# Kernel optimization log

Measured on AMD Instinct MI355X. Metric: run time of the kernel, lower is better.

The kernel has to match this reference:

```python
import jax, jax.numpy as jnp
from jax import lax
import numpy as np

WIDTH = 3.0        # tool half-width (voxels)
SIGMA = 1.0        # soft mask edge (voxels)
BLUR_SIGMA = 1.5   # post-deposit isotropic blur sigma (voxels)
EPS = 1e-8


def _gauss_blur(x, sigma):
    """Separable Gaussian blur over the last two axes of x: [B, X, Y]."""
    radius = int(3 * sigma)
    t = jnp.arange(-radius, radius + 1, dtype=x.dtype)
    k = jnp.exp(-0.5 * (t / sigma) ** 2)
    k = k / k.sum()
    x4 = x[:, None]                      # [B,1,X,Y] NCHW
    kh = k.reshape(1, 1, -1, 1)
    x4 = lax.conv_general_dilated(x4, kh, (1, 1), 'SAME')
    kw = k.reshape(1, 1, 1, -1)
    x4 = lax.conv_general_dilated(x4, kw, (1, 1), 'SAME')
    return x4[:, 0]


def setup_inputs() -> dict:
    key = jax.random.key(0)
    k1, k2, k3 = jax.random.split(key, 3)
    B, H, W = 16, 1024, 1024
    occ = jax.random.uniform(k1, (B, H, W), dtype=jnp.float32)
    # push start/end points well inside the grid (voxel coordinates)
    action_start = jax.random.uniform(k2, (B, 3), minval=200.0, maxval=800.0, dtype=jnp.float32)
    action_end = action_start + jax.random.uniform(k3, (B, 3), minval=-150.0, maxval=150.0, dtype=jnp.float32)
    return {"occ": occ, "action_start": action_start, "action_end": action_end}


def reference(occ, action_start, action_end):
    # coordinate-convention transpose (see SplatPushModel docs)
    rho = jnp.swapaxes(occ, 1, 2)            # [B, X, Y]
    B, X, Y = rho.shape
    p0 = action_start[:, :2]                 # [B,2]
    p1 = action_end[:, :2]                   # [B,2]

    d = p1 - p0
    L = jnp.sqrt(jnp.sum(d * d, axis=-1) + EPS)      # [B] segment length
    u = d / L[:, None]                               # unit push direction
    n = jnp.stack([-u[:, 1], u[:, 0]], axis=-1)      # unit normal

    gx = jnp.arange(X, dtype=rho.dtype)[None, :, None]   # [1,X,1]
    gy = jnp.arange(Y, dtype=rho.dtype)[None, None, :]   # [1,1,Y]
    bc = lambda v: v[:, None, None]                      # [B] -> [B,1,1]

    # --- swept band: soft distance-to-segment mask ---
    rx = gx - bc(p0[:, 0])
    ry = gy - bc(p0[:, 1])
    t = jnp.clip(rx * bc(u[:, 0]) + ry * bc(u[:, 1]), 0.0, L[:, None, None])
    dx = rx - t * bc(u[:, 0])
    dy = ry - t * bc(u[:, 1])
    dist = jnp.sqrt(dx * dx + dy * dy + EPS)
    swept = jax.nn.sigmoid((WIDTH - dist) / SIGMA)       # [B,X,Y]

    m_swept = jnp.sum(rho * swept, axis=(1, 2))          # [B] mass to move
    pile_depth = m_swept / (2.0 * WIDTH)                 # [B]

    # --- landing zone probe (rectangle past p1) ---
    qx = gx - bc(p1[:, 0])
    qy = gy - bc(p1[:, 1])
    s = qx * bc(u[:, 0]) + qy * bc(u[:, 1])              # along-direction coord
    r = qx * bc(n[:, 0]) + qy * bc(n[:, 1])              # perpendicular coord
    lat = jax.nn.sigmoid((WIDTH - jnp.abs(r)) / SIGMA)
    probe = jax.nn.sigmoid(s / SIGMA) * jax.nn.sigmoid((bc(pile_depth) - s) / SIGMA) * lat
    existing = jnp.sum(rho * probe, axis=(1, 2))         # [B]
    extra = existing / (2.0 * WIDTH)                     # [B] forward extension

    # --- deposit band, shifted forward by extra_depth ---
    dep_mask = (jax.nn.sigmoid((s - bc(extra)) / SIGMA)
                * jax.nn.sigmoid((bc(extra) + bc(pile_depth) - s) / SIGMA)
                * lat)
    dep_norm = m_swept / (jnp.sum(dep_mask, axis=(1, 2)) + EPS)
    dep = dep_mask * dep_norm[:, None, None]             # mass-conserving deposit

    if BLUR_SIGMA > 0:
        dep = _gauss_blur(dep, BLUR_SIGMA)

    rho_new = rho * (1.0 - swept) + dep
    return jnp.swapaxes(rho_new, 1, 2)
```

## Files before the change

kernel.cpp:

```cpp
#include <hip/hip_runtime.h>
#include <math.h>

#define BB    16
#define HH    1024
#define WW    1024
#define EPSF  1e-8f
#define RAD   4
#define MARG  24.f
#define NB1   128
#define NB2   64
#define NB3   32
#define WMAX  128
#define FW    (WMAX + 16)

struct BlurK { float k[9]; };

__device__ __forceinline__ float sigf(float z) {
    z = fmaxf(fminf(z, 40.f), -40.f);
    return 1.f / (1.f + __expf(-z));
}

struct Geom { float p0x, p0y, p1x, p1y, L, ux, uy; };

__device__ __forceinline__ Geom load_geom(const float* as, const float* ae, int b) {
    Geom g;
    g.p0x = as[3 * b];  g.p0y = as[3 * b + 1];
    g.p1x = ae[3 * b];  g.p1y = ae[3 * b + 1];
    float dx = g.p1x - g.p0x, dy = g.p1y - g.p0y;
    g.L  = sqrtf(dx * dx + dy * dy + EPSF);
    g.ux = dx / g.L;  g.uy = dy / g.L;
    return g;
}

__device__ __forceinline__ float sweptf(const Geom& g, float x, float y) {
    float rx = x - g.p0x, ry = y - g.p0y;
    float t  = fminf(fmaxf(rx * g.ux + ry * g.uy, 0.f), g.L);
    float dx = rx - t * g.ux, dy = ry - t * g.uy;
    float dist = sqrtf(dx * dx + dy * dy + EPSF);
    return sigf(3.f - dist);
}

__device__ __forceinline__ void slat(const Geom& g, float x, float y, float& s, float& lat) {
    float qx = x - g.p1x, qy = y - g.p1y;
    s = qx * g.ux + qy * g.uy;
    float r = qx * (-g.uy) + qy * g.ux;
    lat = sigf(3.f - fabsf(r));
}

__device__ __forceinline__ void capsule_bbox(const Geom& g, float m,
                                             int& x0, int& x1, int& y0, int& y1) {
    x0 = max(0, (int)floorf(fminf(g.p0x, g.p1x) - m));
    x1 = min(WW - 1, (int)ceilf(fmaxf(g.p0x, g.p1x) + m));
    y0 = max(0, (int)floorf(fminf(g.p0y, g.p1y) - m));
    y1 = min(HH - 1, (int)ceilf(fmaxf(g.p0y, g.p1y) + m));
}

__device__ __forceinline__ void strip_bbox(const Geom& g, float s0, float s1, float m,
                                           int& x0, int& x1, int& y0, int& y1) {
    float xmin = 1e9f, xmax = -1e9f, ymin = 1e9f, ymax = -1e9f;
    #pragma unroll
    for (int i = 0; i < 4; i++) {
        float s = (i & 1) ? s1 : s0;
        float r = (i & 2) ? m : -m;
        float x = g.p1x + s * g.ux - r * g.uy;
        float y = g.p1y + s * g.uy + r * g.ux;
        xmin = fminf(xmin, x); xmax = fmaxf(xmax, x);
        ymin = fminf(ymin, y); ymax = fmaxf(ymax, y);
    }
    x0 = max(0, (int)floorf(xmin)); x1 = min(WW - 1, (int)ceilf(xmax));
    y0 = max(0, (int)floorf(ymin)); y1 = min(HH - 1, (int)ceilf(ymax));
}

__device__ __forceinline__ bool ivx(float a, float A, float B, float& lo, float& hi) {
    if (fabsf(a) < 1e-5f) return !(A > 0.f || B < 0.f);
    float l = A / a, h = B / a;
    if (a < 0.f) { float t = l; l = h; h = t; }
    lo = fmaxf(lo, l); hi = fminf(hi, h);
    return true;
}

__device__ __forceinline__ float brb256(float v, float* sm) {
    #pragma unroll
    for (int off = 32; off > 0; off >>= 1) v += __shfl_down(v, off);
    const int lane = threadIdx.x & 63, wid = threadIdx.x >> 6;
    if (lane == 0) sm[wid] = v;
    __syncthreads();
    float r = sm[0] + sm[1] + sm[2] + sm[3];
    __syncthreads();
    return r;
}

__global__ __launch_bounds__(256)
void k_main(const float* __restrict__ occ, const float* __restrict__ as,
            const float* __restrict__ ae, float* __restrict__ out,
            float* __restrict__ part1) {
    const int b = blockIdx.y, bx = blockIdx.x, tid = threadIdx.x;
    Geom g = load_geom(as, ae, b);
    const size_t ibase = (size_t)b << 20;
    const float4* src = (const float4*)(occ + ibase);
    float4*       dst = (float4*)(out + ibase);
    const int yb = bx * 8;
    const int base4 = bx * 2048 + tid;

    float4 v[8];
    #pragma unroll
    for (int k = 0; k < 8; k++) v[k] = src[base4 + k * 256];

    int cx0, cx1, cy0, cy1; capsule_bbox(g, MARG, cx0, cx1, cy0, cy1);
    const int x = tid << 2;
    float msum = 0.f;
    if (x + 3 >= cx0 && x <= cx1) {
        #pragma unroll
        for (int k = 0; k < 8; k++) {
            const int y = yb + k;
            if (y >= cy0 && y <= cy1) {
                const float fy = (float)y, fx = (float)x;
                const float s0 = sweptf(g, fx + 0.f, fy);
                const float s1 = sweptf(g, fx + 1.f, fy);
                const float s2 = sweptf(g, fx + 2.f, fy);
                const float s3 = sweptf(g, fx + 3.f, fy);
                msum += v[k].x * s0 + v[k].y * s1 + v[k].z * s2 + v[k].w * s3;
                v[k].x *= 1.f - s0; v[k].y *= 1.f - s1;
                v[k].z *= 1.f - s2; v[k].w *= 1.f - s3;
            }
        }
    }
    #pragma unroll
    for (int k = 0; k < 8; k++) dst[base4 + k * 256] = v[k];

    __shared__ float sm[4];
    const float bs = brb256(msum, sm);
    if (tid == 0) part1[b * NB1 + bx] = bs;
}

__global__ __launch_bounds__(256)
void k_existing(const float* __restrict__ occ, const float* __restrict__ as,
                const float* __restrict__ ae, const float* __restrict__ part1,
                float* __restrict__ part2) {
    const int b = blockIdx.y, bx = blockIdx.x, tid = threadIdx.x;
    __shared__ float sm[4];
    const float m_swept = brb256((tid < NB1) ? part1[b * NB1 + tid] : 0.f, sm);
    const float pile = m_swept * (1.f / 6.f);

    Geom g = load_geom(as, ae, b);
    int x0, x1, y0, y1; strip_bbox(g, -MARG, pile + MARG, MARG, x0, x1, y0, y1);
    const float* base = occ + ((size_t)b << 20);
    float sum = 0.f;
    for (int y = y0 + bx; y <= y1; y += NB2) {
        const float fy = (float)y;
        for (int x = x0 + tid; x <= x1; x += 256) {
            float s, lat; slat(g, (float)x, fy, s, lat);
            sum += base[((size_t)y << 10) + x] * sigf(s) * sigf(pile - s) * lat;
        }
    }
    const float bs = brb256(sum, sm);
    if (tid == 0) part2[b * NB2 + bx] = bs;
}

__global__ __launch_bounds__(256)
void k_summask(const float* __restrict__ as, const float* __restrict__ ae,
               const float* __restrict__ part1, const float* __restrict__ part2,
               float* __restrict__ part3) {
    const int b = blockIdx.y, bx = blockIdx.x, tid = threadIdx.x;
    __shared__ float sm[4];
    const float m_swept  = brb256((tid < NB1) ? part1[b * NB1 + tid] : 0.f, sm);
    const float existing = brb256((tid < NB2) ? part2[b * NB2 + tid] : 0.f, sm);
    const float pile  = m_swept * (1.f / 6.f);
    const float extra = existing * (1.f / 6.f);

    Geom g = load_geom(as, ae, b);
    int x0, x1, y0, y1;
    strip_bbox(g, extra - MARG, extra + pile + MARG, MARG, x0, x1, y0, y1);
    float sum = 0.f;
    for (int y = y0 + bx; y <= y1; y += NB2) {
        const float fy = (float)y;
        for (int x = x0 + tid; x <= x1; x += 256) {
            float s, lat; slat(g, (float)x, fy, s, lat);
            sum += sigf(s - extra) * sigf(extra + pile - s) * lat;
        }
    }
    const float bs = brb256(sum, sm);
    if (tid == 0) part3[b * NB2 + bx] = bs;
}

__global__ __launch_bounds__(256)
void k_dep(const float* __restrict__ as, const float* __restrict__ ae,
           const float* __restrict__ part1, const float* __restrict__ part2,
           const float* __restrict__ part3, float* __restrict__ out, BlurK wk) {
    const int b = blockIdx.y, bx = blockIdx.x, tid = threadIdx.x;
    __shared__ float sm[4];
    const float m_swept  = brb256((tid < NB1) ? part1[b * NB1 + tid] : 0.f, sm);
    const float existing = brb256((tid < NB2) ? part2[b * NB2 + tid] : 0.f, sm);
    const float summask  = brb256((tid < NB2) ? part3[b * NB2 + tid] : 0.f, sm);
    const float pile     = m_swept * (1.f / 6.f);
    const float extra    = existing * (1.f / 6.f);
    const float dep_norm = m_swept / (summask + EPSF);

    Geom g = load_geom(as, ae, b);
    int sx0, sx1, sy0, sy1;
    strip_bbox(g, extra - MARG, extra + pile + MARG, MARG, sx0, sx1, sy0, sy1);
    if (sx0 > sx1 || sy0 > sy1) return;
    float* outb = out + ((size_t)b << 20);

    __shared__ float draw[16][FW];
    __shared__ float hb[16][WMAX];

    const int nty = (sy1 - sy0) / 8 + 1;
    const float sA = extra - MARG, sB = extra + pile + MARG;

    for (int ty = bx; ty < nty; ty += NB3) {
        const int yt = sy0 + ty * 8;

        float xlo = 1e9f, xhi = -1e9f;
        #pragma unroll
        for (int r = 0; r < 16; r++) {
            const float dy = (float)(yt - RAD + r) - g.p1y;
            float lo = -1e9f, hi = 1e9f;
            bool ok = ivx(g.ux, sA - dy * g.uy, sB - dy * g.uy, lo, hi);
            ok = ok && ivx(-g.uy, -MARG - dy * g.ux, MARG - dy * g.ux, lo, hi);
            if (ok && lo <= hi) { xlo = fminf(xlo, lo); xhi = fmaxf(xhi, hi); }
        }
        const int csx0 = max(sx0, (int)floorf(xlo + g.p1x));
        const int csx1 = min(sx1, (int)ceilf(xhi + g.p1x));
        if (csx0 > csx1) continue;

        for (int cx = csx0 & ~3; cx <= csx1; cx += WMAX) {
            const int w = min(WMAX, csx1 - cx + 1);

            for (int i = tid; i < 16 * FW; i += 256) {
                const int ly = i / FW, lx = i - ly * FW;
                if (lx < w + 8) {
                    const int gy = yt - RAD + ly, gx = cx - RAD + lx;
                    float val = 0.f;
                    if ((unsigned)gx < WW && (unsigned)gy < HH) {
                        float s, lat; slat(g, (float)gx, (float)gy, s, lat);
                        val = sigf(s - extra) * sigf(extra + pile - s) * lat * dep_norm;
                    }
                    draw[ly][lx] = val;
                }
            }
            __syncthreads();

            for (int i = tid; i < 16 * WMAX; i += 256) {
                const int ly = i >> 7, lx = i & 127;
                if (lx < w) {
                    float acc = 0.f;
                    #pragma unroll
                    for (int j = 0; j < 9; j++) acc += wk.k[j] * draw[ly][lx + j];
                    hb[ly][lx] = acc;
                }
            }
            __syncthreads();

            for (int i = tid; i < 8 * WMAX; i += 256) {
                const int k = i >> 7, lx = i & 127;
                if (lx < w) {
                    float acc = 0.f;
                    #pragma unroll
                    for (int j = 0; j < 9; j++) acc += wk.k[j] * hb[k + j][lx];
                    draw[k][lx] = acc;
                }
            }
            __syncthreads();

            for (int i = tid; i < 8 * WMAX; i += 256) {
                const int k = i >> 7, lx = i & 127;
                const int gy = yt + k, gx = cx + lx;
                if (lx < w && (unsigned)gy < HH && (unsigned)gx < WW)
                    outb[((size_t)gy << 10) + gx] += draw[k][lx];
            }
            __syncthreads();
        }
    }
}

extern "C" void kernel_launch(void* const* d_in, const int* in_sizes, int n_in,
                              void* d_out, int out_size, void* d_ws, size_t ws_size,
                              hipStream_t stream) {
    const float* occ = (const float*)d_in[0];
    const float* as  = (const float*)d_in[1];
    const float* ae  = (const float*)d_in[2];
    float* out   = (float*)d_out;
    float* part1 = (float*)d_ws;
    float* part2 = part1 + BB * NB1;
    float* part3 = part2 + BB * NB2;

    BlurK wk;
    {
        float s = 0.f;
        for (int i = 0; i < 9; i++) {
            float t = (float)(i - RAD) / 1.5f;
            wk.k[i] = expf(-0.5f * t * t);
            s += wk.k[i];
        }
        for (int i = 0; i < 9; i++) wk.k[i] /= s;
    }

    k_main    <<<dim3(NB1, BB), 256, 0, stream>>>(occ, as, ae, out, part1);
    k_existing<<<dim3(NB2, BB), 256, 0, stream>>>(occ, as, ae, part1, part2);
    k_summask <<<dim3(NB2, BB), 256, 0, stream>>>(as, ae, part1, part2, part3);
    k_dep     <<<dim3(NB3, BB), 256, 0, stream>>>(as, ae, part1, part2, part3, out, wk);
}
```

Measured before the change: 136.3 us.

## Fuse existing-mass and mask-sum reductions into deposit kernel with per-row clipping

Merges the k_existing and k_summask reductions into k_dep, so every block of k_dep redundantly computes the landing-zone probe sum and the deposit-mask sum on its own. This removes two kernel launches and the partial-sum round trips through workspace memory. It also adds per-row x clipping of the rotated strip, so only pixels inside the band are visited rather than the whole axis-aligned bounding box. The cost is that 32 blocks per batch each repeat both reductions serially, which adds latency before the blur and deposit stage.

```diff
diff --git a/kernel.cpp b/kernel.cpp
--- a/kernel.cpp
+++ b/kernel.cpp
@@ -8,7 +8,6 @@
 #define RAD   4
 #define MARG  24.f
 #define NB1   128
-#define NB2   64
 #define NB3   32
 #define WMAX  128
 #define FW    (WMAX + 16)
@@ -77,6 +76,18 @@
     if (a < 0.f) { float t = l; l = h; h = t; }
     lo = fmaxf(lo, l); hi = fminf(hi, h);
     return true;
+}
+
+__device__ __forceinline__ bool row_clip(const Geom& g, float fy, float sA, float sB,
+                                         int& xa, int& xb) {
+    const float dy = fy - g.p1y;
+    float lo = -1e9f, hi = 1e9f;
+    bool ok = ivx(g.ux, sA - dy * g.uy, sB - dy * g.uy, lo, hi);
+    ok = ok && ivx(-g.uy, -MARG - dy * g.ux, MARG - dy * g.ux, lo, hi);
+    if (!ok || lo > hi) return false;
+    xa = max(0, (int)floorf(lo + g.p1x));
+    xb = min(WW - 1, (int)ceilf(hi + g.p1x));
+    return xa <= xb;
 }
 
 __device__ __forceinline__ float brb256(float v, float* sm) {
@@ -134,71 +145,49 @@
 }
 
 __global__ __launch_bounds__(256)
-void k_existing(const float* __restrict__ occ, const float* __restrict__ as,
-                const float* __restrict__ ae, const float* __restrict__ part1,
-                float* __restrict__ part2) {
+void k_dep(const float* __restrict__ occ, const float* __restrict__ as,
+           const float* __restrict__ ae, const float* __restrict__ part1,
+           float* __restrict__ out, BlurK wk) {
     const int b = blockIdx.y, bx = blockIdx.x, tid = threadIdx.x;
+    const int lane = tid & 63, wv = tid >> 6;
     __shared__ float sm[4];
+    Geom g = load_geom(as, ae, b);
+    const float* ob = occ + ((size_t)b << 20);
+
     const float m_swept = brb256((tid < NB1) ? part1[b * NB1 + tid] : 0.f, sm);
     const float pile = m_swept * (1.f / 6.f);
 
-    Geom g = load_geom(as, ae, b);
-    int x0, x1, y0, y1; strip_bbox(g, -MARG, pile + MARG, MARG, x0, x1, y0, y1);
-    const float* base = occ + ((size_t)b << 20);
+    int x0, x1, y0, y1;
+    strip_bbox(g, -MARG, pile + MARG, MARG, x0, x1, y0, y1);
     float sum = 0.f;
-    for (int y = y0 + bx; y <= y1; y += NB2) {
+    for (int y = y0 + wv; y <= y1; y += 4) {
         const float fy = (float)y;
-        for (int x = x0 + tid; x <= x1; x += 256) {
-            float s, lat; slat(g, (float)x, fy, s, lat);
-            sum += base[((size_t)y << 10) + x] * sigf(s) * sigf(pile - s) * lat;
-        }
-    }
-    const float bs = brb256(sum, sm);
-    if (tid == 0) part2[b * NB2 + bx] = bs;
-}
-
-__global__ __launch_bounds__(256)
-void k_summask(const float* __restrict__ as, const float* __restrict__ ae,
-               const float* __restrict__ part1, const float* __restrict__ part2,
-               float* __restrict__ part3) {
-    const int b = blockIdx.y, bx = blockIdx.x, tid = threadIdx.x;
-    __shared__ float sm[4];
-    const float m_swept  = brb256((tid < NB1) ? part1[b * NB1 + tid] : 0.f, sm);
-    const float existing = brb256((tid < NB2) ? part2[b * NB2 + tid] : 0.f, sm);
-    const float pile  = m_swept * (1.f / 6.f);
+        int xa, xb;
+        if (!row_clip(g, fy, -MARG, pile + MARG, xa, xb)) continue;
+        for (int xx = xa + lane; xx <= xb; xx += 64) {
+            float s, lat; slat(g, (float)xx, fy, s, lat);
+            sum += ob[((size_t)y << 10) + xx] * sigf(s) * sigf(pile - s) * lat;
+        }
+    }
+    const float existing = brb256(sum, sm);
     const float extra = existing * (1.f / 6.f);
 
-    Geom g = load_geom(as, ae, b);
-    int x0, x1, y0, y1;
-    strip_bbox(g, extra - MARG, extra + pile + MARG, MARG, x0, x1, y0, y1);
-    float sum = 0.f;
-    for (int y = y0 + bx; y <= y1; y += NB2) {
+    const float sA = extra - MARG, sB = extra + pile + MARG;
+    int sx0, sx1, sy0, sy1;
+    strip_bbox(g, sA, sB, MARG, sx0, sx1, sy0, sy1);
+    sum = 0.f;
+    for (int y = sy0 + wv; y <= sy1; y += 4) {
         const float fy = (float)y;
-        for (int x = x0 + tid; x <= x1; x += 256) {
-            float s, lat; slat(g, (float)x, fy, s, lat);
+        int xa, xb;
+        if (!row_clip(g, fy, sA, sB, xa, xb)) continue;
+        for (int xx = xa + lane; xx <= xb; xx += 64) {
+            float s, lat; slat(g, (float)xx, fy, s, lat);
             sum += sigf(s - extra) * sigf(extra + pile - s) * lat;
         }
     }
-    const float bs = brb256(sum, sm);
-    if (tid == 0) part3[b * NB2 + bx] = bs;
-}
-
-__global__ __launch_bounds__(256)
-void k_dep(const float* __restrict__ as, const float* __restrict__ ae,
-           const float* __restrict__ part1, const float* __restrict__ part2,
-           const float* __restrict__ part3, float* __restrict__ out, BlurK wk) {
-    const int b = blockIdx.y, bx = blockIdx.x, tid = threadIdx.x;
-    __shared__ float sm[4];
-    const float m_swept  = brb256((tid < NB1) ? part1[b * NB1 + tid] : 0.f, sm);
-    const float existing = brb256((tid < NB2) ? part2[b * NB2 + tid] : 0.f, sm);
-    const float summask  = brb256((tid < NB2) ? part3[b * NB2 + tid] : 0.f, sm);
-    const float pile     = m_swept * (1.f / 6.f);
-    const float extra    = existing * (1.f / 6.f);
+    const float summask = brb256(sum, sm);
     const float dep_norm = m_swept / (summask + EPSF);
 
-    Geom g = load_geom(as, ae, b);
-    int sx0, sx1, sy0, sy1;
-    strip_bbox(g, extra - MARG, extra + pile + MARG, MARG, sx0, sx1, sy0, sy1);
     if (sx0 > sx1 || sy0 > sy1) return;
     float* outb = out + ((size_t)b << 20);
 
@@ -206,7 +195,6 @@
     __shared__ float hb[16][WMAX];
 
     const int nty = (sy1 - sy0) / 8 + 1;
-    const float sA = extra - MARG, sB = extra + pile + MARG;
 
     for (int ty = bx; ty < nty; ty += NB3) {
         const int yt = sy0 + ty * 8;
@@ -282,8 +270,6 @@
     const float* ae  = (const float*)d_in[2];
     float* out   = (float*)d_out;
     float* part1 = (float*)d_ws;
-    float* part2 = part1 + BB * NB1;
-    float* part3 = part2 + BB * NB2;
 
     BlurK wk;
     {
@@ -296,8 +282,6 @@
         for (int i = 0; i < 9; i++) wk.k[i] /= s;
     }
 
-    k_main    <<<dim3(NB1, BB), 256, 0, stream>>>(occ, as, ae, out, part1);
-    k_existing<<<dim3(NB2, BB), 256, 0, stream>>>(occ, as, ae, part1, part2);
-    k_summask <<<dim3(NB2, BB), 256, 0, stream>>>(as, ae, part1, part2, part3);
-    k_dep     <<<dim3(NB3, BB), 256, 0, stream>>>(as, ae, part1, part2, part3, out, wk);
-}
+    k_main<<<dim3(NB1, BB), 256, 0, stream>>>(occ, as, ae, out, part1);
+    k_dep <<<dim3(NB3, BB), 256, 0, stream>>>(occ, as, ae, part1, out, wk);
+}
```

Result: slower. 167.6 us (+23.0%).
